# Optimization experiments

Measured on AMD Instinct MI355X. Metric: run time of the kernel, lower is better.

Reference implementation:

```python
import jax, jax.numpy as jnp
import numpy as np

B, S, HID = 2, 2048, 2048
H = 16
HD = HID // H            # 128
HD2 = HD // 2            # 64 (rope dim per head)
LAT = HID // 8           # 256 latent dim
BASE = 10000.0


def _rotary_table(seq_len):
    # inv_freq over rope dim HD2
    inv_freq = 1.0 / (BASE ** (jnp.arange(0, HD2, 2, dtype=jnp.float32) / HD2))  # [HD2//2]
    pos = jnp.arange(seq_len, dtype=jnp.float32)
    sincos = pos[:, None] * inv_freq[None, :]                 # [S, HD2//2]
    return jnp.concatenate([jnp.sin(sincos), jnp.cos(sincos)], axis=-1)  # [S, HD2]


def _apply_rope(x, emb):
    # x: [B, S, H, HD2]; emb: [S, HD2]
    half = HD2 // 2
    x1, x2 = x[..., :half], x[..., half:]
    sin = emb[None, :, None, :half]
    cos = emb[None, :, None, half:]
    return jnp.concatenate([x1 * cos - x2 * sin, x1 * sin + x2 * cos], axis=-1)


def setup_inputs() -> dict:
    key = jax.random.key(0)
    ks = jax.random.split(key, 9)
    s = 0.02
    return {
        "hidden_states": jax.random.normal(ks[0], (B, S, HID), jnp.float32),
        "w_kv_d": jax.random.normal(ks[1], (HID, LAT), jnp.float32) * s,
        "w_q_d": jax.random.normal(ks[2], (HID, LAT), jnp.float32) * s,
        "w_k_u": jax.random.normal(ks[3], (LAT, H * HD2), jnp.float32) * s,
        "w_q_u": jax.random.normal(ks[4], (LAT, H * HD2), jnp.float32) * s,
        "w_v_u": jax.random.normal(ks[5], (LAT, H * HD), jnp.float32) * s,
        "w_rope_k": jax.random.normal(ks[6], (HID, HID // 2), jnp.float32) * s,
        "w_rope_q": jax.random.normal(ks[7], (LAT, HID // 2), jnp.float32) * s,
        "w_o": jax.random.normal(ks[8], (HID, HID), jnp.float32) * s,
    }


def reference(hidden_states, w_kv_d, w_q_d, w_k_u, w_q_u, w_v_u, w_rope_k, w_rope_q, w_o):
    b, s, _ = hidden_states.shape
    kv_d = hidden_states @ w_kv_d            # [B,S,LAT]
    q_d = hidden_states @ w_q_d              # [B,S,LAT]
    k_p = (kv_d @ w_k_u).reshape(b, s, H, HD2)
    q_p = (q_d @ w_q_u).reshape(b, s, H, HD2)
    v = (kv_d @ w_v_u).reshape(b, s, H, HD)
    k_r = (hidden_states @ w_rope_k).reshape(b, s, H, HD2)
    q_r = (q_d @ w_rope_q).reshape(b, s, H, HD2)

    emb = _rotary_table(s)
    k_r = _apply_rope(k_r, emb)
    q_r = _apply_rope(q_r, emb)

    k = jnp.concatenate([k_p, k_r], axis=-1)  # [B,S,H,HD]
    q = jnp.concatenate([q_p, q_r], axis=-1)

    scores = jnp.einsum('bqhd,bkhd->bhqk', q, k) / jnp.sqrt(jnp.float32(HD))
    causal = jnp.tril(jnp.ones((s, s), dtype=bool))
    scores = jnp.where(causal[None, None], scores, jnp.float32(-1e9))
    probs = jax.nn.softmax(scores, axis=-1)
    out = jnp.einsum('bhqk,bkhd->bqhd', probs, v).reshape(b, s, HID)
    return out @ w_o
```

## Files before the change

### kernel.cpp

```cpp
#include <hip/hip_runtime.h>
#include <hip/hip_bf16.h>

#define BB 2
#define SS 2048
#define HID 2048
#define NH 16
#define BS (BB*SS)
#define SCALE 0.088388347648318447f
#define C2LOG 0.12751743f

typedef __bf16 bf16x8 __attribute__((ext_vector_type(8)));
typedef float f32x4 __attribute__((ext_vector_type(4)));
typedef float f32x16 __attribute__((ext_vector_type(16)));
typedef unsigned int uintx2 __attribute__((ext_vector_type(2)));

__device__ __forceinline__ bf16x8 ld_frag(const __hip_bfloat16* p) {
    uint4 u = *reinterpret_cast<const uint4*>(p);
    return __builtin_bit_cast(bf16x8, u);
}
__device__ __forceinline__ void store_c(__hip_bfloat16* C, size_t idx, float v) {
    C[idx] = __float2bfloat16(v);
}
__device__ __forceinline__ void store_c(float* C, size_t idx, float v) {
    C[idx] = v;
}
__device__ __forceinline__ ushort bf_bits(float v) {
    __hip_bfloat16 h = __float2bfloat16(v);
    return *reinterpret_cast<ushort*>(&h);
}

#define GLD16(gp, lp) \
  __builtin_amdgcn_global_load_lds((const __attribute__((address_space(1))) void*)(gp), \
                                   (__attribute__((address_space(3))) void*)(lp), 16, 0, 0)

__global__ __launch_bounds__(256) void convert_kernel(
    const float* __restrict__ src, __hip_bfloat16* __restrict__ dst, int n8)
{
    int i = blockIdx.x * blockDim.x + threadIdx.x;
    if (i >= n8) return;
    float4 a = reinterpret_cast<const float4*>(src)[2 * i];
    float4 b = reinterpret_cast<const float4*>(src)[2 * i + 1];
    ushort u[8] = { bf_bits(a.x), bf_bits(a.y), bf_bits(a.z), bf_bits(a.w),
                    bf_bits(b.x), bf_bits(b.y), bf_bits(b.z), bf_bits(b.w) };
    reinterpret_cast<uint4*>(dst)[i] = *reinterpret_cast<uint4*>(u);
}

__global__ __launch_bounds__(256) void transpose_weights_kernel(
    const float* s0, const float* s1, const float* s2, const float* s3,
    const float* s4, const float* s5, const float* s6, const float* s7,
    __hip_bfloat16* WT1, __hip_bfloat16* WT2, __hip_bfloat16* WT3,
    __hip_bfloat16* WTo)
{
    const float* srcs[8] = { s0, s1, s2, s3, s4, s5, s6, s7 };
    const int Rs[8] = { 2048, 2048, 2048, 256, 256, 256, 256, 2048 };
    const int Cs[8] = { 256, 256, 1024, 1024, 2048, 1024, 1024, 2048 };
    __hip_bfloat16* dsts[8] = {
        WT1, WT1 + (size_t)256 * 2048, WT1 + (size_t)512 * 2048,
        WT2, WT2 + (size_t)1024 * 256,
        WT3, WT3 + (size_t)1024 * 256,
        WTo };
    const int prefix[9] = { 0, 512, 1024, 3072, 3328, 3840, 4096, 4352, 8448 };

    int bid = blockIdx.x;
    int seg = 0;
    #pragma unroll
    for (int i = 0; i < 8; i++) if (bid >= prefix[i + 1]) seg = i + 1;
    int local = bid - prefix[seg];
    int R = Rs[seg], C = Cs[seg];
    int tilesC = C / 32;
    int tr = local / tilesC, tc = local % tilesC;
    int r0 = tr * 32, c0 = tc * 32;
    const float* src = srcs[seg];
    __hip_bfloat16* dst = dsts[seg];

    __shared__ float Ts[32][33];
    int t = threadIdx.x;
    int ty = t >> 5, tx = t & 31;
    #pragma unroll
    for (int k = 0; k < 4; k++) {
        int r = ty + k * 8;
        Ts[r][tx] = src[(size_t)(r0 + r) * C + c0 + tx];
    }
    __syncthreads();
    #pragma unroll
    for (int k = 0; k < 4; k++) {
        int r = ty + k * 8;
        dst[(size_t)(c0 + r) * R + r0 + tx] = __float2bfloat16(Ts[tx][r]);
    }
}

template <typename TC>
__global__ __launch_bounds__(256) void gemm_bt_kernel(
    const __hip_bfloat16* __restrict__ A, int lda,
    const __hip_bfloat16* __restrict__ Bt,
    TC* __restrict__ C0, int ldc0, int sp0, int off0, float cm0,
    TC* __restrict__ C1, int ldc1, int sp1, int off1, float cm1,
    int splitN, int K)
{
    __shared__ alignas(16) __hip_bfloat16 As[128 * 32];
    __shared__ alignas(16) __hip_bfloat16 Bs[128 * 32];

    const int bn = blockIdx.x * 128;
    const int bm = blockIdx.y * 128;
    const int t = threadIdx.x;
    const int w = t >> 6;
    const int lane = t & 63;
    const int l15 = lane & 15;
    const int quad = lane >> 4;
    const int wm = (w & 1) * 64;
    const int wn = (w >> 1) * 64;

    const int srow = lane >> 2;
    const int skcol = (lane & 3) * 8;

    f32x4 acc[4][4] = {};

    for (int k0 = 0; k0 < K; k0 += 32) {
        __syncthreads();
        #pragma unroll
        for (int i = 0; i < 2; i++) {
            int r = w * 32 + i * 16 + srow;
            GLD16(A + (size_t)(bm + r) * lda + k0 + skcol, &As[r * 32 + skcol]);
            GLD16(Bt + (size_t)(bn + r) * K + k0 + skcol, &Bs[r * 32 + skcol]);
        }
        __syncthreads();

        bf16x8 af[4], bf[4];
        #pragma unroll
        for (int mt = 0; mt < 4; mt++)
            af[mt] = ld_frag(&As[(wm + mt * 16 + l15) * 32 + quad * 8]);
        #pragma unroll
        for (int nt = 0; nt < 4; nt++)
            bf[nt] = ld_frag(&Bs[(wn + nt * 16 + l15) * 32 + quad * 8]);
        #pragma unroll
        for (int mt = 0; mt < 4; mt++)
            #pragma unroll
            for (int nt = 0; nt < 4; nt++)
                acc[mt][nt] = __builtin_amdgcn_mfma_f32_16x16x32_bf16(
                    af[mt], bf[nt], acc[mt][nt], 0, 0, 0);
    }

    #pragma unroll
    for (int nt = 0; nt < 4; nt++) {
        int col = bn + wn + nt * 16 + l15;
        TC* Cp; int c, ld, s64, off; float cm;
        if (col < splitN) { Cp = C0; c = col; ld = ldc0; s64 = sp0; off = off0; cm = cm0; }
        else { Cp = C1; c = col - splitN; ld = ldc1; s64 = sp1; off = off1; cm = cm1; }
        if (s64 == 2) {
            #pragma unroll
            for (int mt = 0; mt < 4; mt++) {
                int row0 = bm + wm + mt * 16 + quad * 4;
                #pragma unroll
                for (int r = 0; r < 4; r++)
                    store_c(Cp, (size_t)c * 4096 + row0 + r, acc[mt][nt][r] * cm);
            }
        } else {
            int oc = s64 ? ((c >> 6) * 128 + (c & 63) + off) : c;
            #pragma unroll
            for (int mt = 0; mt < 4; mt++) {
                #pragma unroll
                for (int r = 0; r < 4; r++) {
                    int row = bm + wm + mt * 16 + quad * 4 + r;
                    store_c(Cp, (size_t)row * ld + oc, acc[mt][nt][r] * cm);
                }
            }
        }
    }
}

__global__ __launch_bounds__(256) void rope_kernel(
    __hip_bfloat16* __restrict__ Kb, __hip_bfloat16* __restrict__ Qb)
{
    int idx = blockIdx.x * blockDim.x + threadIdx.x;
    if (idx >= BS * NH * 32) return;
    int i = idx & 31;
    int h = (idx >> 5) & 15;
    int row = idx >> 9;
    int s = row & (SS - 1);

    float inv = exp2f(-(float)i * 0.4152410118609203f);
    float ang = (float)s * inv;
    float sn = sinf(ang), cs = cosf(ang);

    size_t obase = (size_t)row * 2048 + h * 128 + 64 + i;
    {
        float x1 = __bfloat162float(Kb[obase]);
        float x2 = __bfloat162float(Kb[obase + 32]);
        Kb[obase]      = __float2bfloat16(x1 * cs - x2 * sn);
        Kb[obase + 32] = __float2bfloat16(x1 * sn + x2 * cs);
    }
    {
        float x1 = __bfloat162float(Qb[obase]);
        float x2 = __bfloat162float(Qb[obase + 32]);
        Qb[obase]      = __float2bfloat16(x1 * cs - x2 * sn);
        Qb[obase + 32] = __float2bfloat16(x1 * sn + x2 * cs);
    }
}

__global__ __launch_bounds__(512) void flash_attn_kernel(
    const __hip_bfloat16* __restrict__ Q,
    const __hip_bfloat16* __restrict__ Kb,
    const __hip_bfloat16* __restrict__ Vt,
    __hip_bfloat16* __restrict__ O)
{
    __shared__ alignas(16) __hip_bfloat16 Ktd[2 * 4 * 64 * 32];
    __shared__ alignas(16) __hip_bfloat16 Vsd[2 * 2 * 128 * 32];

    const int p = blockIdx.x;
    const int h = blockIdx.y;
    const int b = blockIdx.z;
    const int t = threadIdx.x;
    const int w = t >> 6;
    const int lane = t & 63;
    const int l31 = lane & 31;
    const int hi = lane >> 5;
    const int swl = (l31 >> 1) & 3;

    const int qt = (w < 4) ? (15 - p) : p;
    const int wq = w & 3;
    const int qwb = qt * 128 + wq * 32;
    const int q = qwb + l31;
    const int my_nt = 2 * qt + 1 + (wq >> 1);
    const int nbig = 2 * (15 - p) + 2;

    const __hip_bfloat16* Kbase = Kb + (size_t)(b * SS) * 2048 + h * 128;
    const __hip_bfloat16* Vtb = Vt + (size_t)(h * 128) * 4096 + b * SS;

    bf16x8 qf[8];
    {
        const __hip_bfloat16* qrow = Q + (size_t)(b * SS + q) * 2048 + h * 128;
        #pragma unroll
        for (int s = 0; s < 8; s++)
            qf[s] = ld_frag(qrow + s * 16 + hi * 8);
    }

    const int Lr = lane >> 2;
    const int Lc = (lane & 3) ^ ((lane >> 3) & 3);
    const int kds = w >> 1, khalf = w & 1;
    const int vkvh = w >> 2, vdq = w & 3;

    float m_i = -INFINITY;
    float l_i = 0.0f;
    f32x16 acc[4] = {};

    #pragma unroll
    for (int i = 0; i < 2; i++)
        GLD16(Kbase + (size_t)(khalf * 32 + i * 16 + Lr) * 2048 + kds * 32 + Lc * 8,
              &Ktd[kds * 2048 + khalf * 1024 + i * 512 + lane * 8]);
    #pragma unroll
    for (int i = 0; i < 2; i++)
        GLD16(Vtb + (size_t)(vdq * 32 + i * 16 + Lr) * 4096 + vkvh * 32 + Lc * 8,
              &Vsd[vkvh * 4096 + vdq * 1024 + i * 512 + lane * 8]);
    asm volatile("" :: "v"(qf[0]), "v"(qf[1]), "v"(qf[2]), "v"(qf[3]),
                       "v"(qf[4]), "v"(qf[5]), "v"(qf[6]), "v"(qf[7]));

    for (int kt = 0; kt < nbig; kt++) {
        const int kvb = kt * 64;
        const int par = kt & 1;
        const bool active = (kt < my_nt);

        __builtin_amdgcn_s_barrier();
        asm volatile("" ::: "memory");

        {
            const int kvb1 = ((kt + 1 < nbig) ? kt + 1 : kt) * 64;
            const int pn = (par ^ 1) * 8192;
            #pragma unroll
            for (int i = 0; i < 2; i++)
                GLD16(Kbase + (size_t)(kvb1 + khalf * 32 + i * 16 + Lr) * 2048
                          + kds * 32 + Lc * 8,
                      &Ktd[pn + kds * 2048 + khalf * 1024 + i * 512 + lane * 8]);
            #pragma unroll
            for (int i = 0; i < 2; i++)
                GLD16(Vtb + (size_t)(vdq * 32 + i * 16 + Lr) * 4096
                          + kvb1 + vkvh * 32 + Lc * 8,
                      &Vsd[pn + vkvh * 4096 + vdq * 1024 + i * 512 + lane * 8]);
        }
        asm volatile("s_waitcnt vmcnt(4)" ::: "memory");
        __builtin_amdgcn_s_barrier();
        asm volatile("" ::: "memory");

        if (active) {
            const __hip_bfloat16* kb_base = &Ktd[par * 8192];
            const __hip_bfloat16* vb_base = &Vsd[par * 8192];

            f32x16 st[2] = {};
            __builtin_amdgcn_s_setprio(1);
            #pragma unroll
            for (int s = 0; s < 8; s++)
                #pragma unroll
                for (int kb = 0; kb < 2; kb++) {
                    bf16x8 kf = ld_frag(kb_base + (s >> 1) * 2048 + (kb * 32 + l31) * 32
                                        + ((2 * (s & 1) + hi) ^ swl) * 8);
                    st[kb] = __builtin_amdgcn_mfma_f32_32x32x16_bf16(
                        kf, qf[s], st[kb], 0, 0, 0);
                }
            __builtin_amdgcn_s_setprio(0);

            float tmx = -INFINITY;
            if (kvb + 63 > qwb) {
                const int thr = q - kvb - 4 * hi;
                #pragma unroll
                for (int kb = 0; kb < 2; kb++)
                    #pragma unroll
                    for (int g = 0; g < 4; g++)
                        #pragma unroll
                        for (int r = 0; r < 4; r++) {
                            const int e = g * 4 + r;
                            float v = (kb * 32 + 8 * g + r <= thr) ? st[kb][e] : -INFINITY;
                            st[kb][e] = v;
                            tmx = fmaxf(tmx, v);
                        }
            } else {
                #pragma unroll
                for (int kb = 0; kb < 2; kb++)
                    #pragma unroll
                    for (int e = 0; e < 16; e++)
                        tmx = fmaxf(tmx, st[kb][e]);
            }
            tmx = fmaxf(tmx, __shfl_xor(tmx, 32));
            const float m2x = tmx * C2LOG;

            const bool nosc = __all(m2x <= m_i + 8.0f);
            const float mnew = nosc ? m_i : fmaxf(m_i, m2x);
            float rs = 0.0f;
            #pragma unroll
            for (int kb = 0; kb < 2; kb++)
                #pragma unroll
                for (int e = 0; e < 16; e++) {
                    float pv = exp2f(fmaf(st[kb][e], C2LOG, -mnew));
                    st[kb][e] = pv;
                    rs += pv;
                }
            rs += __shfl_xor(rs, 32);
            if (!nosc) {
                const float alpha = exp2f(m_i - mnew);
                m_i = mnew;
                l_i *= alpha;
                #pragma unroll
                for (int dt = 0; dt < 4; dt++)
                    #pragma unroll
                    for (int e = 0; e < 16; e++)
                        acc[dt][e] *= alpha;
            }
            l_i += rs;

            uint4 af[4];
            #pragma unroll
            for (int kb = 0; kb < 2; kb++) {
                unsigned int pk[4][2];
                #pragma unroll
                for (int g = 0; g < 4; g++)
                    #pragma unroll
                    for (int i = 0; i < 2; i++) {
                        float2 fp = make_float2(st[kb][g * 4 + 2 * i],
                                                st[kb][g * 4 + 2 * i + 1]);
                        __hip_bfloat162 h2 = __float22bfloat162_rn(fp);
                        pk[g][i] = *reinterpret_cast<unsigned int*>(&h2);
                    }
                #pragma unroll
                for (int sl = 0; sl < 2; sl++) {
                    uintx2 r0 = __builtin_amdgcn_permlane32_swap(
                        pk[2 * sl][0], pk[2 * sl + 1][0], false, false);
                    uintx2 r1 = __builtin_amdgcn_permlane32_swap(
                        pk[2 * sl][1], pk[2 * sl + 1][1], false, false);
                    af[kb * 2 + sl] = make_uint4(r0[0], r1[0], r0[1], r1[1]);
                }
            }

            __builtin_amdgcn_s_setprio(1);
            #pragma unroll
            for (int s = 0; s < 4; s++) {
                bf16x8 pf = __builtin_bit_cast(bf16x8, af[s]);
                #pragma unroll
                for (int dt = 0; dt < 4; dt++) {
                    bf16x8 vf = ld_frag(vb_base + (s >> 1) * 4096 + (dt * 32 + l31) * 32
                                        + ((2 * (s & 1) + hi) ^ swl) * 8);
                    acc[dt] = __builtin_amdgcn_mfma_f32_32x32x16_bf16(
                        vf, pf, acc[dt], 0, 0, 0);
                }
            }
            __builtin_amdgcn_s_setprio(0);
        }
    }

    const float inv_l = 1.0f / l_i;
    __hip_bfloat16* orow = O + (size_t)(b * SS + q) * 2048 + h * 128;
    #pragma unroll
    for (int dt = 0; dt < 4; dt++)
        #pragma unroll
        for (int g = 0; g < 4; g++) {
            ushort u[4];
            #pragma unroll
            for (int r = 0; r < 4; r++)
                u[r] = bf_bits(acc[dt][g * 4 + r] * inv_l);
            *reinterpret_cast<uint2*>(orow + dt * 32 + 8 * g + 4 * hi) =
                *reinterpret_cast<uint2*>(u);
        }
}

extern "C" void kernel_launch(void* const* d_in, const int* in_sizes, int n_in,
                              void* d_out, int out_size, void* d_ws, size_t ws_size,
                              hipStream_t stream)
{
    const float* hs       = (const float*)d_in[0];
    const float* w_kv_d   = (const float*)d_in[1];
    const float* w_q_d    = (const float*)d_in[2];
    const float* w_k_u    = (const float*)d_in[3];
    const float* w_q_u    = (const float*)d_in[4];
    const float* w_v_u    = (const float*)d_in[5];
    const float* w_rope_k = (const float*)d_in[6];
    const float* w_rope_q = (const float*)d_in[7];
    const float* w_o      = (const float*)d_in[8];
    float* out = (float*)d_out;

    char* p = (char*)d_ws;
    auto alloc = [&](size_t nelem) {
        __hip_bfloat16* r = (__hip_bfloat16*)p;
        p += nelem * sizeof(__hip_bfloat16);
        return r;
    };
    __hip_bfloat16* hsb  = alloc((size_t)BS * HID);
    __hip_bfloat16* qkvd = alloc((size_t)BS * 512);
    __hip_bfloat16* WT1  = alloc((size_t)1536 * 2048);
    __hip_bfloat16* WT2  = alloc((size_t)3072 * 256);
    __hip_bfloat16* WT3  = alloc((size_t)2048 * 256);
    __hip_bfloat16* WTo  = alloc((size_t)2048 * 2048);
    __hip_bfloat16* Kbuf = alloc((size_t)BS * HID);
    __hip_bfloat16* Qbuf = alloc((size_t)BS * HID);
    __hip_bfloat16* Vtb  = alloc((size_t)HID * BS);
    __hip_bfloat16* attn = hsb;

    dim3 blk(256);

    convert_kernel<<<dim3((BS * HID / 8 + 255) / 256), blk, 0, stream>>>(
        hs, hsb, BS * HID / 8);
    transpose_weights_kernel<<<dim3(8448), blk, 0, stream>>>(
        w_kv_d, w_q_d, w_rope_k, w_k_u, w_v_u, w_q_u, w_rope_q, w_o,
        WT1, WT2, WT3, WTo);

    gemm_bt_kernel<__hip_bfloat16><<<dim3(1536 / 128, BS / 128), blk, 0, stream>>>(
        hsb, 2048, WT1,
        qkvd, 512, 0, 0, 1.0f,
        Kbuf, 2048, 1, 64, 1.0f,
        512, 2048);
    gemm_bt_kernel<__hip_bfloat16><<<dim3(3072 / 128, BS / 128), blk, 0, stream>>>(
        qkvd, 512, WT2,
        Kbuf, 2048, 1, 0, 1.0f,
        Vtb, 0, 2, 0, 1.0f,
        1024, 256);
    gemm_bt_kernel<__hip_bfloat16><<<dim3(2048 / 128, BS / 128), blk, 0, stream>>>(
        qkvd + 256, 512, WT3,
        Qbuf, 2048, 1, 0, 1.0f,
        Qbuf, 2048, 1, 64, 1.0f,
        1024, 256);
    rope_kernel<<<dim3((BS * NH * 32 + 255) / 256), blk, 0, stream>>>(Kbuf, Qbuf);
    flash_attn_kernel<<<dim3(8, NH, BB), dim3(512), 0, stream>>>(
        Qbuf, Kbuf, Vtb, attn);
    gemm_bt_kernel<float><<<dim3(2048 / 128, BS / 128), blk, 0, stream>>>(
        attn, 2048, WTo,
        out, 2048, 0, 0, 1.0f,
        out, 2048, 0, 0, 1.0f,
        2048, 2048);
}
```

Baseline: 347.6 us.

## Store K/V tiles in LDS in fragment-major order and swizzle GEMM block order

```diff
diff --git a/kernel.cpp b/kernel.cpp
--- a/kernel.cpp
+++ b/kernel.cpp
@@ -100,8 +100,12 @@
     __shared__ alignas(16) __hip_bfloat16 As[128 * 32];
     __shared__ alignas(16) __hip_bfloat16 Bs[128 * 32];
 
-    const int bn = blockIdx.x * 128;
-    const int bm = blockIdx.y * 128;
+    const int nwg = gridDim.x * gridDim.y;
+    int lin = blockIdx.y * gridDim.x + blockIdx.x;
+    lin = (lin & 7) * (nwg >> 3) + (lin >> 3);
+    const int bn = (lin % gridDim.x) * 128;
+    const int bm = (lin / gridDim.x) * 128;
+
     const int t = threadIdx.x;
     const int w = t >> 6;
     const int lane = t & 63;
@@ -203,8 +207,8 @@
     const __hip_bfloat16* __restrict__ Vt,
     __hip_bfloat16* __restrict__ O)
 {
-    __shared__ alignas(16) __hip_bfloat16 Ktd[2 * 4 * 64 * 32];
-    __shared__ alignas(16) __hip_bfloat16 Vsd[2 * 2 * 128 * 32];
+    __shared__ alignas(16) __hip_bfloat16 Ktd[2 * 16 * 512];
+    __shared__ alignas(16) __hip_bfloat16 Vsd[2 * 16 * 512];
 
     const int p = blockIdx.x;
     const int h = blockIdx.y;
@@ -214,7 +218,6 @@
     const int lane = t & 63;
     const int l31 = lane & 31;
     const int hi = lane >> 5;
-    const int swl = (l31 >> 1) & 3;
 
     const int qt = (w < 4) ? (15 - p) : p;
     const int wq = w & 3;
@@ -234,10 +237,11 @@
             qf[s] = ld_frag(qrow + s * 16 + hi * 8);
     }
 
-    const int Lr = lane >> 2;
-    const int Lc = (lane & 3) ^ ((lane >> 3) & 3);
-    const int kds = w >> 1, khalf = w & 1;
-    const int vkvh = w >> 2, vdq = w & 3;
+    const int kb_w = w >> 2, ks0 = (2 * w) & 7;
+    const int dt_w = w >> 1, vs0 = (2 * w) & 3;
+    const size_t kg_l = (size_t)l31 * 2048 + hi * 8;
+    const size_t vg_l = (size_t)(dt_w * 32 + l31) * 4096 + hi * 8;
+    const int loff = lane * 8;
 
     float m_i = -INFINITY;
     float l_i = 0.0f;
@@ -245,12 +249,12 @@
 
     #pragma unroll
     for (int i = 0; i < 2; i++)
-        GLD16(Kbase + (size_t)(khalf * 32 + i * 16 + Lr) * 2048 + kds * 32 + Lc * 8,
-              &Ktd[kds * 2048 + khalf * 1024 + i * 512 + lane * 8]);
+        GLD16(Kbase + (size_t)(kb_w * 32) * 2048 + kg_l + (ks0 + i) * 16,
+              &Ktd[(kb_w * 8 + ks0 + i) * 512 + loff]);
     #pragma unroll
     for (int i = 0; i < 2; i++)
-        GLD16(Vtb + (size_t)(vdq * 32 + i * 16 + Lr) * 4096 + vkvh * 32 + Lc * 8,
-              &Vsd[vkvh * 4096 + vdq * 1024 + i * 512 + lane * 8]);
+        GLD16(Vtb + vg_l + (vs0 + i) * 16,
+              &Vsd[(dt_w * 4 + vs0 + i) * 512 + loff]);
     asm volatile("" :: "v"(qf[0]), "v"(qf[1]), "v"(qf[2]), "v"(qf[3]),
                        "v"(qf[4]), "v"(qf[5]), "v"(qf[6]), "v"(qf[7]));
 
@@ -267,14 +271,12 @@
             const int pn = (par ^ 1) * 8192;
             #pragma unroll
             for (int i = 0; i < 2; i++)
-                GLD16(Kbase + (size_t)(kvb1 + khalf * 32 + i * 16 + Lr) * 2048
-                          + kds * 32 + Lc * 8,
-                      &Ktd[pn + kds * 2048 + khalf * 1024 + i * 512 + lane * 8]);
+                GLD16(Kbase + (size_t)(kvb1 + kb_w * 32) * 2048 + kg_l + (ks0 + i) * 16,
+                      &Ktd[pn + (kb_w * 8 + ks0 + i) * 512 + loff]);
             #pragma unroll
             for (int i = 0; i < 2; i++)
-                GLD16(Vtb + (size_t)(vdq * 32 + i * 16 + Lr) * 4096
-                          + kvb1 + vkvh * 32 + Lc * 8,
-                      &Vsd[pn + vkvh * 4096 + vdq * 1024 + i * 512 + lane * 8]);
+                GLD16(Vtb + vg_l + kvb1 + (vs0 + i) * 16,
+                      &Vsd[pn + (dt_w * 4 + vs0 + i) * 512 + loff]);
         }
         asm volatile("s_waitcnt vmcnt(4)" ::: "memory");
         __builtin_amdgcn_s_barrier();
@@ -290,8 +292,7 @@
             for (int s = 0; s < 8; s++)
                 #pragma unroll
                 for (int kb = 0; kb < 2; kb++) {
-                    bf16x8 kf = ld_frag(kb_base + (s >> 1) * 2048 + (kb * 32 + l31) * 32
-                                        + ((2 * (s & 1) + hi) ^ swl) * 8);
+                    bf16x8 kf = ld_frag(kb_base + (kb * 8 + s) * 512 + loff);
                     st[kb] = __builtin_amdgcn_mfma_f32_32x32x16_bf16(
                         kf, qf[s], st[kb], 0, 0, 0);
                 }
@@ -374,8 +375,7 @@
                 bf16x8 pf = __builtin_bit_cast(bf16x8, af[s]);
                 #pragma unroll
                 for (int dt = 0; dt < 4; dt++) {
-                    bf16x8 vf = ld_frag(vb_base + (s >> 1) * 4096 + (dt * 32 + l31) * 32
-                                        + ((2 * (s & 1) + hi) ^ swl) * 8);
+                    bf16x8 vf = ld_frag(vb_base + (dt * 4 + s) * 512 + loff);
                     acc[dt] = __builtin_amdgcn_mfma_f32_32x32x16_bf16(
                         vf, pf, acc[dt], 0, 0, 0);
                 }
```

After: 351.3 us. About the same (+1.0%).
